# Kernel optimization log

Hardware: AMD Instinct MI355X
Metric: run time of the kernel (lower is better)

Reference implementation:

```python
import jax, jax.numpy as jnp
import numpy as np

N_NODES = 50000
N_EDGES = 1600000


def gcn_conv(x, edge_index, W, b):
    """PyG GCNConv: linear transform, add self-loops, symmetric deg^-1/2 norm, scatter-add."""
    n = x.shape[0]
    h = x @ W  # [N, out]
    loop = jnp.arange(n)
    src = jnp.concatenate([edge_index[0], loop])
    dst = jnp.concatenate([edge_index[1], loop])
    ones = jnp.ones(src.shape[0], dtype=h.dtype)
    deg = jax.ops.segment_sum(ones, dst, num_segments=n)  # in-degree incl. self-loop
    dinv = jnp.where(deg > 0, jax.lax.rsqrt(deg), 0.0)
    norm = dinv[src] * dinv[dst]  # [E+N]
    msg = h[src] * norm[:, None]  # gathered, normalized messages
    out = jax.ops.segment_sum(msg, dst, num_segments=n)
    return out + b


def setup_inputs() -> dict:
    key = jax.random.key(0)
    k1, k2, k3, k4 = jax.random.split(key, 4)
    x = jax.random.normal(k1, (N_NODES, 512), dtype=jnp.float32)
    edge_index = jax.random.randint(k2, (2, N_EDGES), 0, N_NODES, dtype=jnp.int64)
    W1 = jax.random.normal(k3, (512, 128), dtype=jnp.float32) * (1.0 / np.sqrt(512))
    b1 = jnp.zeros((128,), dtype=jnp.float32)
    W2 = jax.random.normal(k4, (128, 40), dtype=jnp.float32) * (1.0 / np.sqrt(128))
    b2 = jnp.zeros((40,), dtype=jnp.float32)
    return {"x": x, "edge_index": edge_index, "W1": W1, "b1": b1, "W2": W2, "b2": b2}


def reference(x, edge_index, W1, b1, W2, b2):
    h = gcn_conv(x, edge_index, W1, b1)
    h = jax.nn.relu(h)
    h = gcn_conv(h, edge_index, W2, b2)
    return jax.nn.log_softmax(h, axis=1)
```

## Files before the change

### kernel.cpp

```cpp
#include <hip/hip_runtime.h>
#include <hip/hip_bf16.h>
#include <math.h>


#define FEAT1 512
#define FEAT2 128
#define FEAT3 40

typedef __attribute__((ext_vector_type(8))) short bf16x8;
typedef __attribute__((ext_vector_type(4))) float f32x4;

__device__ __forceinline__ unsigned short f2bf(float f) {
    union { float f; unsigned u; } c; c.f = f;
    unsigned r = c.u + 0x7fff + ((c.u >> 16) & 1);
    return (unsigned short)(r >> 16);
}
__device__ __forceinline__ float bf2f(unsigned v16) {
    union { unsigned u; float f; } c; c.u = v16 << 16;
    return c.f;
}

__device__ __forceinline__ bf16x8 pack_bf8(f32x4 a, f32x4 b) {
    union { __hip_bfloat162 h[4]; bf16x8 v; } u;
    u.h[0] = __float22bfloat162_rn(make_float2(a[0], a[1]));
    u.h[1] = __float22bfloat162_rn(make_float2(a[2], a[3]));
    u.h[2] = __float22bfloat162_rn(make_float2(b[0], b[1]));
    u.h[3] = __float22bfloat162_rn(make_float2(b[2], b[3]));
    return u.v;
}

__global__ void detect_i64_kernel(const int* __restrict__ ei, int* flagp) {
    __shared__ int any;
    if (threadIdx.x == 0) any = 0;
    __syncthreads();
    int v = ei[2 * threadIdx.x + 1];
    if (v != 0) any = 1;
    __syncthreads();
    if (threadIdx.x == 0) *flagp = (any == 0) ? 1 : 0;
}

__device__ __forceinline__ int load_src(const int* ei, long e, long E, int f64) {
    return f64 ? ei[2 * e] : ei[e];
}
__device__ __forceinline__ int load_dst(const int* ei, long e, long E, int f64) {
    return f64 ? ei[2 * E + 2 * e] : ei[E + e];
}

__launch_bounds__(1024)
__global__ void partA_kernel(const int* __restrict__ ei, const int* __restrict__ flagp,
                             int* __restrict__ gbkt, unsigned* __restrict__ part,
                             int bktCap, long E, int NB) {
    __shared__ int hist[256], lbase[256], lcur[256];
    int f64 = *flagp;
    int t = threadIdx.x;
    long chunk = (E + gridDim.x - 1) / gridDim.x;
    long start = (long)blockIdx.x * chunk;
    long end = start + chunk; if (end > E) end = E;
    if (t < 256) { hist[t] = 0; lcur[t] = 0; }
    __syncthreads();

    for (long e0 = start; e0 < end; e0 += 1024) {
        long e = e0 + t;
        if (e < end) {
            int dst = load_dst(ei, e, E, f64);
            atomicAdd(&hist[dst >> 8], 1);
        }
    }
    __syncthreads();
    if (t < NB && hist[t]) lbase[t] = atomicAdd(&gbkt[t], hist[t]);
    __syncthreads();

    for (long e0 = start; e0 < end; e0 += 1024) {
        long e = e0 + t;
        if (e < end) {
            int src = load_src(ei, e, E, f64);
            int dst = load_dst(ei, e, E, f64);
            int bkt = dst >> 8;
            int pos = lbase[bkt] + atomicAdd(&lcur[bkt], 1);
            if (pos < bktCap)
                part[(long)bkt * bktCap + pos] = (unsigned)src | ((unsigned)(dst & 255) << 17);
        }
    }
}

__global__ void bscan_kernel(const int* __restrict__ gbkt, int* __restrict__ bktBase,
                             int* __restrict__ offsets, int NB, int N, int E) {
    __shared__ int s[256];
    int t = threadIdx.x;
    int v = (t < NB) ? gbkt[t] : 0;
    s[t] = v;
    __syncthreads();
    #pragma unroll
    for (int d = 1; d < 256; d <<= 1) {
        int tv = (t >= d) ? s[t - d] : 0;
        __syncthreads();
        s[t] += tv;
        __syncthreads();
    }
    bktBase[t] = s[t] - v;
    if (t == 0) offsets[N] = E;
}

__launch_bounds__(256)
__global__ void partB_kernel(const unsigned* __restrict__ part, int bktCap,
                             const int* __restrict__ gbkt, const int* __restrict__ bktBase,
                             int* __restrict__ offsets, float* __restrict__ dinv,
                             int* __restrict__ col, int N) {
    __shared__ int h[256], sc[256], cur[256];
    int b = blockIdx.x, t = threadIdx.x;
    int n = gbkt[b]; if (n > bktCap) n = bktCap;
    int base = bktBase[b];
    int lo = b << 8;
    const unsigned* p = part + (long)b * bktCap;
    h[t] = 0;
    __syncthreads();
    for (int i = t; i < n; i += 256) atomicAdd(&h[(p[i] >> 17) & 255], 1);
    __syncthreads();
    int cnt = h[t];
    sc[t] = cnt;
    __syncthreads();
    #pragma unroll
    for (int d = 1; d < 256; d <<= 1) {
        int tv = (t >= d) ? sc[t - d] : 0;
        __syncthreads();
        sc[t] += tv;
        __syncthreads();
    }
    int ex = sc[t] - cnt;
    int node = lo + t;
    if (node < N) {
        offsets[node] = base + ex;
        dinv[node] = 1.0f / sqrtf((float)(cnt + 1));
    }
    cur[t] = ex;
    __syncthreads();
    for (int i = t; i < n; i += 256) {
        unsigned u = p[i];
        int r = atomicAdd(&cur[(u >> 17) & 255], 1);
        col[base + r] = u & 0x1FFFF;
    }
}

__global__ void w1bt_kernel(const float* __restrict__ W1, unsigned short* __restrict__ Bt) {
    int r = blockIdx.x;
    int x7 = r & 7;
    for (int k = threadIdx.x; k < FEAT1; k += blockDim.x) {
        int c = k >> 3, j = k & 7;
        int eo = (((c ^ x7) << 3) | j);
        Bt[(long)r * FEAT1 + eo] = f2bf(W1[(long)k * FEAT2 + r]);
    }
}

__global__ void w2bt_kernel(const float* __restrict__ W2, unsigned short* __restrict__ Bt2) {
    int n = blockIdx.x;
    for (int k = threadIdx.x; k < FEAT2; k += blockDim.x)
        Bt2[(long)n * FEAT2 + k] = (n < FEAT3) ? f2bf(W2[(long)k * FEAT3 + n]) : 0;
}

#define G1_NW 8
__launch_bounds__(512, 2)
__global__ void gemm1_mfma_kernel(const float* __restrict__ A,
                                  const unsigned short* __restrict__ Bsw,
                                  const float* __restrict__ dinv,
                                  unsigned short* __restrict__ C, int M) {
    __shared__ unsigned short Bl[FEAT2 * FEAT1];
    int t = threadIdx.x;

    {
        uint4 tmp[16];
        #pragma unroll
        for (int r = 0; r < 16; r++)
            tmp[r] = *(const uint4*)((const char*)Bsw + (size_t)t * 16 + (size_t)r * 8192);
        #pragma unroll
        for (int r = 0; r < 16; r++)
            *(uint4*)((char*)Bl + (size_t)t * 16 + (size_t)r * 8192) = tmp[r];
    }
    __syncthreads();

    int wave = blockIdx.x * G1_NW + (t >> 6);
    int lane = t & 63;
    int quad = lane >> 4, r15 = lane & 15;
    int row0 = wave * 16;
    if (row0 < M) {
        int arow = row0 + r15;
        if (arow >= M) arow = M - 1;
        const float* ap = A + (long)arow * FEAT1 + quad * 8;
        int x7 = r15 & 7;

        f32x4 ra[4][2];
        #pragma unroll
        for (int p = 0; p < 3; p++) {
            ra[p][0] = *(const f32x4*)(ap + p * 32);
            ra[p][1] = *(const f32x4*)(ap + p * 32 + 4);
        }

        f32x4 acc[8];
        #pragma unroll
        for (int nt = 0; nt < 8; nt++) acc[nt] = (f32x4){0.f, 0.f, 0.f, 0.f};

        #pragma unroll
        for (int ks = 0; ks < 16; ks++) {
            if (ks < 13) {
                ra[(ks + 3) & 3][0] = *(const f32x4*)(ap + (ks + 3) * 32);
                ra[(ks + 3) & 3][1] = *(const f32x4*)(ap + (ks + 3) * 32 + 4);
            }
            bf16x8 af = pack_bf8(ra[ks & 3][0], ra[ks & 3][1]);
            #pragma unroll
            for (int nt = 0; nt < 8; nt++) {
                int eo = (nt * 16 + r15) * FEAT1 + (((ks * 4 + quad) ^ x7) << 3);
                bf16x8 bfrag = *(const bf16x8*)(Bl + eo);
                acc[nt] = __builtin_amdgcn_mfma_f32_16x16x32_bf16(af, bfrag, acc[nt], 0, 0, 0);
            }
        }

        #pragma unroll
        for (int reg = 0; reg < 4; reg++) {
            int orow = row0 + quad * 4 + reg;
            if (orow < M) {
                float di = dinv[orow];
                #pragma unroll
                for (int nt = 0; nt < 8; nt++)
                    C[(long)orow * FEAT2 + nt * 16 + r15] = f2bf(acc[nt][reg] * di);
            }
        }
    }
}

__launch_bounds__(256)
__global__ void agg1_kernel(const unsigned short* __restrict__ h1s,
                            const int* __restrict__ col, const int* __restrict__ off,
                            const float* __restrict__ dinv, const float* __restrict__ b1,
                            unsigned short* __restrict__ a1, int N) {
    int node = blockIdx.x * 4 + (threadIdx.x >> 6);
    if (node >= N) return;
    int l = threadIdx.x & 63;
    int o0 = off[node], o1 = off[node + 1];
    float ax = 0.f, ay = 0.f;
    for (int base = o0; base < o1; base += 64) {
        int cnt = min(64, o1 - base);
        int myc = (l < cnt) ? col[base + l] : 0;
        int e = 0;
        for (; e + 4 <= cnt; e += 4) {
            int s0 = __shfl(myc, e + 0);
            int s1 = __shfl(myc, e + 1);
            int s2 = __shfl(myc, e + 2);
            int s3 = __shfl(myc, e + 3);
            unsigned p0 = *(const unsigned*)(h1s + (long)s0 * FEAT2 + 2 * l);
            unsigned p1 = *(const unsigned*)(h1s + (long)s1 * FEAT2 + 2 * l);
            unsigned p2 = *(const unsigned*)(h1s + (long)s2 * FEAT2 + 2 * l);
            unsigned p3 = *(const unsigned*)(h1s + (long)s3 * FEAT2 + 2 * l);
            ax += bf2f(p0 & 0xffffu) + bf2f(p1 & 0xffffu) +
                  bf2f(p2 & 0xffffu) + bf2f(p3 & 0xffffu);
            ay += bf2f(p0 >> 16) + bf2f(p1 >> 16) + bf2f(p2 >> 16) + bf2f(p3 >> 16);
        }
        for (; e < cnt; ++e) {
            int s = __shfl(myc, e);
            unsigned p = *(const unsigned*)(h1s + (long)s * FEAT2 + 2 * l);
            ax += bf2f(p & 0xffffu);
            ay += bf2f(p >> 16);
        }
    }
    unsigned pv = *(const unsigned*)(h1s + (long)node * FEAT2 + 2 * l);
    ax += bf2f(pv & 0xffffu);
    ay += bf2f(pv >> 16);
    float di = dinv[node];
    float2 b = *(const float2*)(b1 + 2 * l);
    float vx = ax * di + b.x;
    float vy = ay * di + b.y;
    vx = vx > 0.f ? vx : 0.f;
    vy = vy > 0.f ? vy : 0.f;
    *(unsigned*)(a1 + (long)node * FEAT2 + 2 * l) =
        (unsigned)f2bf(vx) | ((unsigned)f2bf(vy) << 16);
}

__launch_bounds__(256)
__global__ void gemm2_mfma_kernel(const unsigned short* __restrict__ A,
                                  const unsigned short* __restrict__ Bt2,
                                  const float* __restrict__ dinv,
                                  unsigned short* __restrict__ C, int M) {
    int wave = blockIdx.x * (blockDim.x >> 6) + (threadIdx.x >> 6);
    int lane = threadIdx.x & 63;
    int quad = lane >> 4, r15 = lane & 15;
    int row0 = wave * 16;
    if (row0 >= M) return;
    int arow = row0 + r15;
    if (arow >= M) arow = M - 1;

    bf16x8 af[4];
    const unsigned short* ap = A + (long)arow * FEAT2 + quad * 8;
    #pragma unroll
    for (int ks = 0; ks < 4; ks++) af[ks] = *(const bf16x8*)(ap + ks * 32);

    f32x4 acc[3];
    #pragma unroll
    for (int nt = 0; nt < 3; nt++) acc[nt] = (f32x4){0.f, 0.f, 0.f, 0.f};
    #pragma unroll
    for (int ks = 0; ks < 4; ks++) {
        #pragma unroll
        for (int nt = 0; nt < 3; nt++) {
            bf16x8 bf = *(const bf16x8*)(Bt2 + (long)(nt * 16 + r15) * FEAT2 + ks * 32 + quad * 8);
            acc[nt] = __builtin_amdgcn_mfma_f32_16x16x32_bf16(af[ks], bf, acc[nt], 0, 0, 0);
        }
    }

    #pragma unroll
    for (int reg = 0; reg < 4; reg++) {
        int orow = row0 + quad * 4 + reg;
        if (orow >= M) continue;
        float di = dinv[orow];
        #pragma unroll
        for (int nt = 0; nt < 3; nt++) {
            int ocol = nt * 16 + r15;
            if (ocol < FEAT3)
                C[(long)orow * FEAT3 + ocol] = f2bf(acc[nt][reg] * di);
        }
    }
}

__launch_bounds__(256)
__global__ void agg2_lsm_kernel(const unsigned short* __restrict__ h2s,
                                const int* __restrict__ col, const int* __restrict__ off,
                                const float* __restrict__ dinv, const float* __restrict__ b2,
                                float* __restrict__ out, int N) {
    int node = blockIdx.x * 4 + (threadIdx.x >> 6);
    if (node >= N) return;
    int l = threadIdx.x & 63;
    bool act = l < FEAT3 / 2;
    int o0 = off[node], o1 = off[node + 1];
    float ax = 0.f, ay = 0.f;
    for (int base = o0; base < o1; base += 64) {
        int cnt = min(64, o1 - base);
        int myc = (l < cnt) ? col[base + l] : 0;
        int e = 0;
        for (; e + 4 <= cnt; e += 4) {
            int s0 = __shfl(myc, e + 0);
            int s1 = __shfl(myc, e + 1);
            int s2 = __shfl(myc, e + 2);
            int s3 = __shfl(myc, e + 3);
            if (act) {
                unsigned p0 = *(const unsigned*)(h2s + (long)s0 * FEAT3 + 2 * l);
                unsigned p1 = *(const unsigned*)(h2s + (long)s1 * FEAT3 + 2 * l);
                unsigned p2 = *(const unsigned*)(h2s + (long)s2 * FEAT3 + 2 * l);
                unsigned p3 = *(const unsigned*)(h2s + (long)s3 * FEAT3 + 2 * l);
                ax += bf2f(p0 & 0xffffu) + bf2f(p1 & 0xffffu) +
                      bf2f(p2 & 0xffffu) + bf2f(p3 & 0xffffu);
                ay += bf2f(p0 >> 16) + bf2f(p1 >> 16) + bf2f(p2 >> 16) + bf2f(p3 >> 16);
            }
        }
        for (; e < cnt; ++e) {
            int s = __shfl(myc, e);
            if (act) {
                unsigned p = *(const unsigned*)(h2s + (long)s * FEAT3 + 2 * l);
                ax += bf2f(p & 0xffffu);
                ay += bf2f(p >> 16);
            }
        }
    }
    float vx = -INFINITY, vy = -INFINITY;
    if (act) {
        unsigned pv = *(const unsigned*)(h2s + (long)node * FEAT3 + 2 * l);
        float di = dinv[node];
        float2 b = *(const float2*)(b2 + 2 * l);
        vx = (ax + bf2f(pv & 0xffffu)) * di + b.x;
        vy = (ay + bf2f(pv >> 16)) * di + b.y;
    }
    float m = fmaxf(vx, vy);
    #pragma unroll
    for (int o = 32; o >= 1; o >>= 1) m = fmaxf(m, __shfl_xor(m, o));
    float e = act ? (expf(vx - m) + expf(vy - m)) : 0.f;
    #pragma unroll
    for (int o = 32; o >= 1; o >>= 1) e += __shfl_xor(e, o);
    float ls = logf(e);
    if (act) {
        *(float2*)(out + (long)node * FEAT3 + 2 * l) = make_float2(vx - m - ls, vy - m - ls);
    }
}

extern "C" void kernel_launch(void* const* d_in, const int* in_sizes, int n_in,
                              void* d_out, int out_size, void* d_ws, size_t ws_size,
                              hipStream_t stream) {
    const float* x  = (const float*)d_in[0];
    const int*   ei = (const int*)d_in[1];
    const float* W1 = (const float*)d_in[2];
    const float* b1 = (const float*)d_in[3];
    const float* W2 = (const float*)d_in[4];
    const float* b2 = (const float*)d_in[5];
    float* out = (float*)d_out;

    const int  N = in_sizes[0] / FEAT1;
    const long E = in_sizes[1] / 2;

    char* ws = (char*)d_ws;
    size_t off = 0;
    auto alloc = [&](size_t bytes) -> void* {
        off = (off + 255) & ~(size_t)255;
        void* p = ws + off;
        off += bytes;
        return p;
    };
    const int NB = (N + 255) >> 8;
    const int bktCap = (int)(E / NB) + 1024;
    int*   offsets = (int*)alloc((size_t)(N + 1) * 4);
    float* dinv    = (float*)alloc((size_t)N * 4);
    int*   col     = (int*)alloc((size_t)E * 4);
    unsigned short* h1s = (unsigned short*)alloc((size_t)N * FEAT2 * 2);
    unsigned short* a1  = (unsigned short*)alloc((size_t)N * FEAT2 * 2);
    unsigned short* h2s = (unsigned short*)alloc((size_t)N * FEAT3 * 2);
    unsigned short* Bt  = (unsigned short*)alloc((size_t)FEAT2 * FEAT1 * 2);
    unsigned short* Bt2 = (unsigned short*)alloc((size_t)48 * FEAT2 * 2);
    unsigned* part = (unsigned*)alloc((size_t)NB * bktCap * 4);
    int*   gbkt    = (int*)alloc(256 * 4);
    int*   bktBase = (int*)alloc(256 * 4);
    int*   flagp   = (int*)alloc(4);

    detect_i64_kernel<<<1, 256, 0, stream>>>(ei, flagp);
    hipMemsetAsync(gbkt, 0, 256 * 4, stream);
    partA_kernel<<<256, 1024, 0, stream>>>(ei, flagp, gbkt, part, bktCap, E, NB);
    bscan_kernel<<<1, 256, 0, stream>>>(gbkt, bktBase, offsets, NB, N, (int)E);
    partB_kernel<<<NB, 256, 0, stream>>>(part, bktCap, gbkt, bktBase, offsets, dinv, col, N);

    w1bt_kernel<<<FEAT2, 256, 0, stream>>>(W1, Bt);
    w2bt_kernel<<<48, 128, 0, stream>>>(W2, Bt2);
    {
        int waves  = (N + 15) / 16;
        int blocks = (waves + G1_NW - 1) / G1_NW;
        gemm1_mfma_kernel<<<blocks, 512, 0, stream>>>(x, Bt, dinv, h1s, N);
    }
    agg1_kernel<<<(N + 3) / 4, 256, 0, stream>>>(h1s, col, offsets, dinv, b1, a1, N);
    gemm2_mfma_kernel<<<(N / 16 + 3) / 4, 256, 0, stream>>>(a1, Bt2, dinv, h2s, N);
    agg2_lsm_kernel<<<(N + 3) / 4, 256, 0, stream>>>(h2s, col, offsets, dinv, b2, out, N);
}
```

Before: 331.4 us.

## Fuse preprocessing kernels, double GEMM1 row tiles per wave, widen agg1 loads

```diff
diff --git a/kernel.cpp b/kernel.cpp
--- a/kernel.cpp
+++ b/kernel.cpp
@@ -29,16 +29,6 @@
     return u.v;
 }
 
-__global__ void detect_i64_kernel(const int* __restrict__ ei, int* flagp) {
-    __shared__ int any;
-    if (threadIdx.x == 0) any = 0;
-    __syncthreads();
-    int v = ei[2 * threadIdx.x + 1];
-    if (v != 0) any = 1;
-    __syncthreads();
-    if (threadIdx.x == 0) *flagp = (any == 0) ? 1 : 0;
-}
-
 __device__ __forceinline__ int load_src(const int* ei, long e, long E, int f64) {
     return f64 ? ei[2 * e] : ei[e];
 }
@@ -47,17 +37,22 @@
 }
 
 __launch_bounds__(1024)
-__global__ void partA_kernel(const int* __restrict__ ei, const int* __restrict__ flagp,
+__global__ void partA_kernel(const int* __restrict__ ei,
                              int* __restrict__ gbkt, unsigned* __restrict__ part,
                              int bktCap, long E, int NB) {
     __shared__ int hist[256], lbase[256], lcur[256];
-    int f64 = *flagp;
+    __shared__ int anyv;
     int t = threadIdx.x;
+    if (t == 0) anyv = 0;
+    if (t < 256) { hist[t] = 0; lcur[t] = 0; }
+    __syncthreads();
+    if (t < 256 && ei[2 * t + 1] != 0) anyv = 1;
+    __syncthreads();
+    int f64 = (anyv == 0) ? 1 : 0;
+
     long chunk = (E + gridDim.x - 1) / gridDim.x;
     long start = (long)blockIdx.x * chunk;
     long end = start + chunk; if (end > E) end = E;
-    if (t < 256) { hist[t] = 0; lcur[t] = 0; }
-    __syncthreads();
 
     for (long e0 = start; e0 < end; e0 += 1024) {
         long e = e0 + t;
@@ -83,41 +78,16 @@
     }
 }
 
-__global__ void bscan_kernel(const int* __restrict__ gbkt, int* __restrict__ bktBase,
-                             int* __restrict__ offsets, int NB, int N, int E) {
-    __shared__ int s[256];
-    int t = threadIdx.x;
-    int v = (t < NB) ? gbkt[t] : 0;
-    s[t] = v;
-    __syncthreads();
-    #pragma unroll
-    for (int d = 1; d < 256; d <<= 1) {
-        int tv = (t >= d) ? s[t - d] : 0;
-        __syncthreads();
-        s[t] += tv;
-        __syncthreads();
-    }
-    bktBase[t] = s[t] - v;
-    if (t == 0) offsets[N] = E;
-}
-
 __launch_bounds__(256)
 __global__ void partB_kernel(const unsigned* __restrict__ part, int bktCap,
-                             const int* __restrict__ gbkt, const int* __restrict__ bktBase,
+                             const int* __restrict__ gbkt,
                              int* __restrict__ offsets, float* __restrict__ dinv,
-                             int* __restrict__ col, int N) {
+                             int* __restrict__ col, int N, int E) {
     __shared__ int h[256], sc[256], cur[256];
     int b = blockIdx.x, t = threadIdx.x;
-    int n = gbkt[b]; if (n > bktCap) n = bktCap;
-    int base = bktBase[b];
-    int lo = b << 8;
-    const unsigned* p = part + (long)b * bktCap;
-    h[t] = 0;
-    __syncthreads();
-    for (int i = t; i < n; i += 256) atomicAdd(&h[(p[i] >> 17) & 255], 1);
-    __syncthreads();
-    int cnt = h[t];
-    sc[t] = cnt;
+    int NB = gridDim.x;
+
+    sc[t] = (t < NB) ? gbkt[t] : 0;
     __syncthreads();
     #pragma unroll
     for (int d = 1; d < 256; d <<= 1) {
@@ -126,6 +96,26 @@
         sc[t] += tv;
         __syncthreads();
     }
+    int base = (b == 0) ? 0 : sc[b - 1];
+    if (b == 0 && t == 0) offsets[N] = E;
+
+    int n = gbkt[b]; if (n > bktCap) n = bktCap;
+    int lo = b << 8;
+    const unsigned* p = part + (long)b * bktCap;
+    h[t] = 0;
+    __syncthreads();
+    for (int i = t; i < n; i += 256) atomicAdd(&h[(p[i] >> 17) & 255], 1);
+    __syncthreads();
+    int cnt = h[t];
+    sc[t] = cnt;
+    __syncthreads();
+    #pragma unroll
+    for (int d = 1; d < 256; d <<= 1) {
+        int tv = (t >= d) ? sc[t - d] : 0;
+        __syncthreads();
+        sc[t] += tv;
+        __syncthreads();
+    }
     int ex = sc[t] - cnt;
     int node = lo + t;
     if (node < N) {
@@ -141,20 +131,23 @@
     }
 }
 
-__global__ void w1bt_kernel(const float* __restrict__ W1, unsigned short* __restrict__ Bt) {
-    int r = blockIdx.x;
-    int x7 = r & 7;
-    for (int k = threadIdx.x; k < FEAT1; k += blockDim.x) {
-        int c = k >> 3, j = k & 7;
-        int eo = (((c ^ x7) << 3) | j);
-        Bt[(long)r * FEAT1 + eo] = f2bf(W1[(long)k * FEAT2 + r]);
-    }
-}
-
-__global__ void w2bt_kernel(const float* __restrict__ W2, unsigned short* __restrict__ Bt2) {
-    int n = blockIdx.x;
-    for (int k = threadIdx.x; k < FEAT2; k += blockDim.x)
-        Bt2[(long)n * FEAT2 + k] = (n < FEAT3) ? f2bf(W2[(long)k * FEAT3 + n]) : 0;
+__global__ void wbt_kernel(const float* __restrict__ W1, const float* __restrict__ W2,
+                           unsigned short* __restrict__ Bt, unsigned short* __restrict__ Bt2,
+                           int* __restrict__ gbkt) {
+    int b = blockIdx.x;
+    if (b == 0 && threadIdx.x < 256) gbkt[threadIdx.x] = 0;
+    if (b < FEAT2) {
+        int r = b, x7 = r & 7;
+        for (int k = threadIdx.x; k < FEAT1; k += blockDim.x) {
+            int c = k >> 3, j = k & 7;
+            int eo = (((c ^ x7) << 3) | j);
+            Bt[(long)r * FEAT1 + eo] = f2bf(W1[(long)k * FEAT2 + r]);
+        }
+    } else {
+        int n = b - FEAT2;
+        for (int k = threadIdx.x; k < FEAT2; k += blockDim.x)
+            Bt2[(long)n * FEAT2 + k] = (n < FEAT3) ? f2bf(W2[(long)k * FEAT3 + n]) : 0;
+    }
 }
 
 #define G1_NW 8
@@ -177,50 +170,64 @@
     }
     __syncthreads();
 
-    int wave = blockIdx.x * G1_NW + (t >> 6);
-    int lane = t & 63;
+    int w = t >> 6, lane = t & 63;
     int quad = lane >> 4, r15 = lane & 15;
-    int row0 = wave * 16;
-    if (row0 < M) {
-        int arow = row0 + r15;
-        if (arow >= M) arow = M - 1;
-        const float* ap = A + (long)arow * FEAT1 + quad * 8;
-        int x7 = r15 & 7;
-
-        f32x4 ra[4][2];
-        #pragma unroll
-        for (int p = 0; p < 3; p++) {
-            ra[p][0] = *(const f32x4*)(ap + p * 32);
-            ra[p][1] = *(const f32x4*)(ap + p * 32 + 4);
-        }
-
-        f32x4 acc[8];
-        #pragma unroll
-        for (int nt = 0; nt < 8; nt++) acc[nt] = (f32x4){0.f, 0.f, 0.f, 0.f};
-
-        #pragma unroll
-        for (int ks = 0; ks < 16; ks++) {
-            if (ks < 13) {
-                ra[(ks + 3) & 3][0] = *(const f32x4*)(ap + (ks + 3) * 32);
-                ra[(ks + 3) & 3][1] = *(const f32x4*)(ap + (ks + 3) * 32 + 4);
-            }
-            bf16x8 af = pack_bf8(ra[ks & 3][0], ra[ks & 3][1]);
-            #pragma unroll
-            for (int nt = 0; nt < 8; nt++) {
-                int eo = (nt * 16 + r15) * FEAT1 + (((ks * 4 + quad) ^ x7) << 3);
-                bf16x8 bfrag = *(const bf16x8*)(Bl + eo);
-                acc[nt] = __builtin_amdgcn_mfma_f32_16x16x32_bf16(af, bfrag, acc[nt], 0, 0, 0);
-            }
-        }
-
+    int row0 = (blockIdx.x * (G1_NW * 2) + w * 2) * 16;
+    int x7 = r15 & 7;
+
+    int ar0 = row0 + r15;      if (ar0 >= M) ar0 = M - 1;
+    int ar1 = row0 + 16 + r15; if (ar1 >= M) ar1 = M - 1;
+    const float* ap0 = A + (long)ar0 * FEAT1 + quad * 8;
+    const float* ap1 = A + (long)ar1 * FEAT1 + quad * 8;
+
+    f32x4 ra0[3][2], ra1[3][2];
+    #pragma unroll
+    for (int p = 0; p < 3; p++) {
+        ra0[p][0] = *(const f32x4*)(ap0 + p * 32);
+        ra0[p][1] = *(const f32x4*)(ap0 + p * 32 + 4);
+        ra1[p][0] = *(const f32x4*)(ap1 + p * 32);
+        ra1[p][1] = *(const f32x4*)(ap1 + p * 32 + 4);
+    }
+
+    f32x4 acc0[8], acc1[8];
+    #pragma unroll
+    for (int nt = 0; nt < 8; nt++) {
+        acc0[nt] = (f32x4){0.f, 0.f, 0.f, 0.f};
+        acc1[nt] = (f32x4){0.f, 0.f, 0.f, 0.f};
+    }
+
+    #pragma unroll
+    for (int ks = 0; ks < 16; ks++) {
+        int sl = ks % 3;
+        bf16x8 af0 = pack_bf8(ra0[sl][0], ra0[sl][1]);
+        bf16x8 af1 = pack_bf8(ra1[sl][0], ra1[sl][1]);
+        if (ks < 13) {
+            ra0[sl][0] = *(const f32x4*)(ap0 + (ks + 3) * 32);
+            ra0[sl][1] = *(const f32x4*)(ap0 + (ks + 3) * 32 + 4);
+            ra1[sl][0] = *(const f32x4*)(ap1 + (ks + 3) * 32);
+            ra1[sl][1] = *(const f32x4*)(ap1 + (ks + 3) * 32 + 4);
+        }
+        #pragma unroll
+        for (int nt = 0; nt < 8; nt++) {
+            int eo = (nt * 16 + r15) * FEAT1 + (((ks * 4 + quad) ^ x7) << 3);
+            bf16x8 bfrag = *(const bf16x8*)(Bl + eo);
+            acc0[nt] = __builtin_amdgcn_mfma_f32_16x16x32_bf16(af0, bfrag, acc0[nt], 0, 0, 0);
+            acc1[nt] = __builtin_amdgcn_mfma_f32_16x16x32_bf16(af1, bfrag, acc1[nt], 0, 0, 0);
+        }
+    }
+
+    #pragma unroll
+    for (int tile = 0; tile < 2; tile++) {
         #pragma unroll
         for (int reg = 0; reg < 4; reg++) {
-            int orow = row0 + quad * 4 + reg;
+            int orow = row0 + tile * 16 + quad * 4 + reg;
             if (orow < M) {
                 float di = dinv[orow];
                 #pragma unroll
-                for (int nt = 0; nt < 8; nt++)
-                    C[(long)orow * FEAT2 + nt * 16 + r15] = f2bf(acc[nt][reg] * di);
+                for (int nt = 0; nt < 8; nt++) {
+                    float v = (tile == 0) ? acc0[nt][reg] : acc1[nt][reg];
+                    C[(long)orow * FEAT2 + nt * 16 + r15] = f2bf(v * di);
+                }
             }
         }
     }
@@ -234,43 +241,67 @@
     int node = blockIdx.x * 4 + (threadIdx.x >> 6);
     if (node >= N) return;
     int l = threadIdx.x & 63;
+    int h = l >> 5, j = l & 31;
     int o0 = off[node], o1 = off[node + 1];
-    float ax = 0.f, ay = 0.f;
+    float a0 = 0.f, a1f = 0.f, a2 = 0.f, a3 = 0.f;
     for (int base = o0; base < o1; base += 64) {
         int cnt = min(64, o1 - base);
         int myc = (l < cnt) ? col[base + l] : 0;
-        int e = 0;
-        for (; e + 4 <= cnt; e += 4) {
-            int s0 = __shfl(myc, e + 0);
-            int s1 = __shfl(myc, e + 1);
-            int s2 = __shfl(myc, e + 2);
-            int s3 = __shfl(myc, e + 3);
-            unsigned p0 = *(const unsigned*)(h1s + (long)s0 * FEAT2 + 2 * l);
-            unsigned p1 = *(const unsigned*)(h1s + (long)s1 * FEAT2 + 2 * l);
-            unsigned p2 = *(const unsigned*)(h1s + (long)s2 * FEAT2 + 2 * l);
-            unsigned p3 = *(const unsigned*)(h1s + (long)s3 * FEAT2 + 2 * l);
-            ax += bf2f(p0 & 0xffffu) + bf2f(p1 & 0xffffu) +
-                  bf2f(p2 & 0xffffu) + bf2f(p3 & 0xffffu);
-            ay += bf2f(p0 >> 16) + bf2f(p1 >> 16) + bf2f(p2 >> 16) + bf2f(p3 >> 16);
-        }
-        for (; e < cnt; ++e) {
+        int steps = (cnt + 1) >> 1;
+        int i = 0;
+        for (; i + 4 <= steps; i += 4) {
+            int e0 = 2 * (i + 0) + h, e1 = 2 * (i + 1) + h;
+            int e2 = 2 * (i + 2) + h, e3 = 2 * (i + 3) + h;
+            int s0 = __shfl(myc, e0), s1 = __shfl(myc, e1);
+            int s2 = __shfl(myc, e2), s3 = __shfl(myc, e3);
+            if (e0 < cnt) {
+                uint2 p = *(const uint2*)(h1s + (long)s0 * FEAT2 + 4 * j);
+                a0 += bf2f(p.x & 0xffffu); a1f += bf2f(p.x >> 16);
+                a2 += bf2f(p.y & 0xffffu); a3 += bf2f(p.y >> 16);
+            }
+            if (e1 < cnt) {
+                uint2 p = *(const uint2*)(h1s + (long)s1 * FEAT2 + 4 * j);
+                a0 += bf2f(p.x & 0xffffu); a1f += bf2f(p.x >> 16);
+                a2 += bf2f(p.y & 0xffffu); a3 += bf2f(p.y >> 16);
+            }
+            if (e2 < cnt) {
+                uint2 p = *(const uint2*)(h1s + (long)s2 * FEAT2 + 4 * j);
+                a0 += bf2f(p.x & 0xffffu); a1f += bf2f(p.x >> 16);
+                a2 += bf2f(p.y & 0xffffu); a3 += bf2f(p.y >> 16);
+            }
+            if (e3 < cnt) {
+                uint2 p = *(const uint2*)(h1s + (long)s3 * FEAT2 + 4 * j);
+                a0 += bf2f(p.x & 0xffffu); a1f += bf2f(p.x >> 16);
+                a2 += bf2f(p.y & 0xffffu); a3 += bf2f(p.y >> 16);
+            }
+        }
+        for (; i < steps; ++i) {
+            int e = 2 * i + h;
             int s = __shfl(myc, e);
-            unsigned p = *(const unsigned*)(h1s + (long)s * FEAT2 + 2 * l);
-            ax += bf2f(p & 0xffffu);
-            ay += bf2f(p >> 16);
-        }
-    }
-    unsigned pv = *(const unsigned*)(h1s + (long)node * FEAT2 + 2 * l);
-    ax += bf2f(pv & 0xffffu);
-    ay += bf2f(pv >> 16);
-    float di = dinv[node];
-    float2 b = *(const float2*)(b1 + 2 * l);
-    float vx = ax * di + b.x;
-    float vy = ay * di + b.y;
-    vx = vx > 0.f ? vx : 0.f;
-    vy = vy > 0.f ? vy : 0.f;
-    *(unsigned*)(a1 + (long)node * FEAT2 + 2 * l) =
-        (unsigned)f2bf(vx) | ((unsigned)f2bf(vy) << 16);
+            if (e < cnt) {
+                uint2 p = *(const uint2*)(h1s + (long)s * FEAT2 + 4 * j);
+                a0 += bf2f(p.x & 0xffffu); a1f += bf2f(p.x >> 16);
+                a2 += bf2f(p.y & 0xffffu); a3 += bf2f(p.y >> 16);
+            }
+        }
+    }
+    a0 += __shfl_xor(a0, 32); a1f += __shfl_xor(a1f, 32);
+    a2 += __shfl_xor(a2, 32); a3 += __shfl_xor(a3, 32);
+    if (h == 0) {
+        uint2 pv = *(const uint2*)(h1s + (long)node * FEAT2 + 4 * j);
+        a0 += bf2f(pv.x & 0xffffu); a1f += bf2f(pv.x >> 16);
+        a2 += bf2f(pv.y & 0xffffu); a3 += bf2f(pv.y >> 16);
+        float di = dinv[node];
+        float4 b = *(const float4*)(b1 + 4 * j);
+        float v0 = a0 * di + b.x, v1 = a1f * di + b.y;
+        float v2 = a2 * di + b.z, v3 = a3 * di + b.w;
+        v0 = v0 > 0.f ? v0 : 0.f; v1 = v1 > 0.f ? v1 : 0.f;
+        v2 = v2 > 0.f ? v2 : 0.f; v3 = v3 > 0.f ? v3 : 0.f;
+        uint2 o;
+        o.x = (unsigned)f2bf(v0) | ((unsigned)f2bf(v1) << 16);
+        o.y = (unsigned)f2bf(v2) | ((unsigned)f2bf(v3) << 16);
+        *(uint2*)(a1 + (long)node * FEAT2 + 4 * j) = o;
+    }
 }
 
 __launch_bounds__(256)
@@ -410,20 +441,15 @@
     unsigned short* Bt2 = (unsigned short*)alloc((size_t)48 * FEAT2 * 2);
     unsigned* part = (unsigned*)alloc((size_t)NB * bktCap * 4);
     int*   gbkt    = (int*)alloc(256 * 4);
-    int*   bktBase = (int*)alloc(256 * 4);
     int*   flagp   = (int*)alloc(4);
-
-    detect_i64_kernel<<<1, 256, 0, stream>>>(ei, flagp);
-    hipMemsetAsync(gbkt, 0, 256 * 4, stream);
-    partA_kernel<<<256, 1024, 0, stream>>>(ei, flagp, gbkt, part, bktCap, E, NB);
-    bscan_kernel<<<1, 256, 0, stream>>>(gbkt, bktBase, offsets, NB, N, (int)E);
-    partB_kernel<<<NB, 256, 0, stream>>>(part, bktCap, gbkt, bktBase, offsets, dinv, col, N);
-
-    w1bt_kernel<<<FEAT2, 256, 0, stream>>>(W1, Bt);
-    w2bt_kernel<<<48, 128, 0, stream>>>(W2, Bt2);
+    (void)flagp;
+
+    wbt_kernel<<<176, 256, 0, stream>>>(W1, W2, Bt, Bt2, gbkt);
+    partA_kernel<<<256, 1024, 0, stream>>>(ei, gbkt, part, bktCap, E, NB);
+    partB_kernel<<<NB, 256, 0, stream>>>(part, bktCap, gbkt, offsets, dinv, col, N, (int)E);
     {
-        int waves  = (N + 15) / 16;
-        int blocks = (waves + G1_NW - 1) / G1_NW;
+        int tiles  = (N + 15) / 16;
+        int blocks = (tiles + G1_NW * 2 - 1) / (G1_NW * 2);
         gemm1_mfma_kernel<<<blocks, 512, 0, stream>>>(x, Bt, dinv, h1s, N);
     }
     agg1_kernel<<<(N + 3) / 4, 256, 0, stream>>>(h1s, col, offsets, dinv, b1, a1, N);
```

Measured after the change: 332.1 us. No clear change (+0.2%).
